# Performance work log

Hardware: AMD Instinct MI355X
Metric: run time of the kernel (lower is better)

## Reference

```python
import jax, jax.numpy as jnp
import numpy as np

B, T, C = 4, 2048, 1024
NQ, D = 8, C // 8  # n_query heads, head dim = n_embd // 8


def setup_inputs() -> dict:
    key = jax.random.key(0)
    ks = jax.random.split(key, 6)
    s = 0.02
    return {
        "x": jax.random.normal(ks[0], (B, T, C), dtype=jnp.float32),
        "Wk": jax.random.normal(ks[1], (C, D), dtype=jnp.float32) * s,
        "Wv": jax.random.normal(ks[2], (C, D), dtype=jnp.float32) * s,
        "Wq": jax.random.normal(ks[3], (NQ, C, D), dtype=jnp.float32) * s,
        "Wp": jax.random.normal(ks[4], (NQ * D, C), dtype=jnp.float32) * s,
        "bp": jnp.zeros((C,), dtype=jnp.float32),
    }


def reference(x, Wk, Wv, Wq, Wp, bp):
    b, t, c = x.shape
    scale = c ** -0.5  # original scales by n_embd**-0.5, not head-dim
    k = x @ Wk                                   # [B,T,D] shared across heads (MQA)
    v = x @ Wv                                   # [B,T,D]
    q = jnp.einsum("btc,qcd->bqtd", x, Wq)       # [B,NQ,T,D]
    wei = jnp.einsum("bqtd,bsd->bqts", q, k) * scale
    causal = jnp.tril(jnp.ones((t, t), dtype=bool))
    wei = jnp.where(causal, wei, -jnp.inf)
    wei = jax.nn.softmax(wei, axis=-1)
    out = jnp.einsum("bqts,bsd->btqd", wei, v)   # [B,T,NQ,D]
    out = out.reshape(b, t, -1)                  # concat heads -> [B,T,NQ*D]
    return out @ Wp + bp
```

## Files before the change

### kernel.cpp

```cpp
#include <hip/hip_runtime.h>
#include <hip/hip_bf16.h>
#include <cstddef>
#include <cstdint>

#define B 4
#define T 2048
#define C 1024
#define NQ 8
#define D 128
#define M_ROWS (B * T)
#define NTOT (2 * D + NQ * D)

typedef __bf16 bf16x8 __attribute__((ext_vector_type(8)));
typedef float  f32x4  __attribute__((ext_vector_type(4)));
typedef uint32_t u32x4 __attribute__((ext_vector_type(4)));

__device__ __forceinline__ ushort f2bf(float f) {
    union { float f; uint32_t u; } v; v.f = f;
    const uint32_t r = (v.u + 0x7fffu + ((v.u >> 16) & 1u)) >> 16;
    return (ushort)r;
}

__device__ __forceinline__ uint32_t cvt_pk_bf16(float lo, float hi) {
    uint32_t r;
    asm("v_cvt_pk_bf16_f32 %0, %1, %2" : "=v"(r) : "v"(lo), "v"(hi));
    return r;
}

__device__ __forceinline__ void gld_lds16(const ushort* g, ushort* lds_uniform) {
    __builtin_amdgcn_global_load_lds(
        (const __attribute__((address_space(1))) void*)g,
        (__attribute__((address_space(3))) void*)lds_uniform, 16, 0, 0);
}

__global__ __launch_bounds__(256) void xcvt(const float* __restrict__ x,
                                            ushort* __restrict__ xb) {
    const size_t i = ((size_t)blockIdx.x * 256 + threadIdx.x) * 8;
    const float4 a = *(const float4*)(x + i);
    const float4 b = *(const float4*)(x + i + 4);
    uint4 o;
    o.x = f2bf(a.x) | ((uint32_t)f2bf(a.y) << 16);
    o.y = f2bf(a.z) | ((uint32_t)f2bf(a.w) << 16);
    o.z = f2bf(b.x) | ((uint32_t)f2bf(b.y) << 16);
    o.w = f2bf(b.z) | ((uint32_t)f2bf(b.w) << 16);
    *(uint4*)(xb + i) = o;
}

__device__ __forceinline__ void wtrans_body(const float* __restrict__ src,
                                            ushort* __restrict__ dst, int NC,
                                            int bx, int by) {
    __shared__ ushort Ts[64][72];
    const int tid = threadIdx.x;
    const int k0 = by * 64, c0 = bx * 64;
    {
        const int r = tid >> 2, cq = tid & 3;
#pragma unroll
        for (int i = 0; i < 4; ++i) {
            const int cc = cq * 16 + i * 4;
            const float4 v = *(const float4*)(src + (size_t)(k0 + r) * NC + c0 + cc);
            uint2 o;
            o.x = f2bf(v.x) | ((uint32_t)f2bf(v.y) << 16);
            o.y = f2bf(v.z) | ((uint32_t)f2bf(v.w) << 16);
            *(uint2*)(&Ts[r][cc]) = o;
        }
    }
    __syncthreads();
    {
        const int n = tid >> 2, kq = tid & 3;
        ushort vv[16];
#pragma unroll
        for (int j = 0; j < 16; ++j) vv[j] = Ts[kq * 16 + j][n];
        uint4 o0, o1;
        o0.x = vv[0] | ((uint32_t)vv[1] << 16);  o0.y = vv[2] | ((uint32_t)vv[3] << 16);
        o0.z = vv[4] | ((uint32_t)vv[5] << 16);  o0.w = vv[6] | ((uint32_t)vv[7] << 16);
        o1.x = vv[8] | ((uint32_t)vv[9] << 16);  o1.y = vv[10] | ((uint32_t)vv[11] << 16);
        o1.z = vv[12] | ((uint32_t)vv[13] << 16); o1.w = vv[14] | ((uint32_t)vv[15] << 16);
        ushort* d = dst + (size_t)(c0 + n) * C + k0 + kq * 16;
        *(uint4*)d = o0;
        *(uint4*)(d + 8) = o1;
    }
}

__global__ __launch_bounds__(256) void wtrans_qkv(const float* __restrict__ Wk,
                                                  const float* __restrict__ Wv,
                                                  const float* __restrict__ Wq,
                                                  ushort* __restrict__ WcatT) {
    const int z = blockIdx.z;
    const float* src;
    int rbase;
    if (z == 0)      { src = Wk; rbase = 0; }
    else if (z == 1) { src = Wv; rbase = D; }
    else             { src = Wq + (size_t)(z - 2) * C * D; rbase = 2 * D + (z - 2) * D; }
    wtrans_body(src, WcatT + (size_t)rbase * C, D, blockIdx.x, blockIdx.y);
}

__global__ __launch_bounds__(256) void wtrans_p(const float* __restrict__ Wp,
                                                ushort* __restrict__ WpT) {
    wtrans_body(Wp, WpT, C, blockIdx.x, blockIdx.y);
}

__global__ __launch_bounds__(256) void vtrans(const ushort* __restrict__ qkv,
                                              ushort* __restrict__ vbT) {
    __shared__ ushort Ts[64][136];
    const int tid = threadIdx.x;
    const int kb0 = blockIdx.x * 64;
    {
        const int r = tid >> 2, cq = tid & 3;
        const ushort* src = qkv + (size_t)(kb0 + r) * NTOT + D;
#pragma unroll
        for (int i = 0; i < 4; ++i) {
            const int cc = (cq * 4 + i) * 8;
            *(uint4*)(&Ts[r][cc]) = *(const uint4*)(src + cc);
        }
    }
    __syncthreads();
    {
        const int d = tid >> 1, half = tid & 1;
        ushort vv[32];
#pragma unroll
        for (int k = 0; k < 32; ++k) vv[k] = Ts[half * 32 + k][d];
        uint32_t dw[16];
#pragma unroll
        for (int i = 0; i < 16; ++i) {
            const int p0 = 2 * i, p1 = 2 * i + 1;
            const int k0 = (p0 & 3) | (((p0 >> 3) & 3) << 2) | (((p0 >> 2) & 1) << 4);
            const int k1 = (p1 & 3) | (((p1 >> 3) & 3) << 2) | (((p1 >> 2) & 1) << 4);
            dw[i] = vv[k0] | ((uint32_t)vv[k1] << 16);
        }
        uint32_t* dst = (uint32_t*)(vbT + (size_t)d * M_ROWS + kb0 + half * 32);
#pragma unroll
        for (int i = 0; i < 4; ++i)
            *(uint4*)(dst + i * 4) = *(uint4*)(&dw[i * 4]);
    }
}

template <bool BF16_OUT>
__global__ __launch_bounds__(256) void gemm_mfma(const ushort* __restrict__ A,
                                                 const ushort* __restrict__ Bt,
                                                 void* __restrict__ Cout,
                                                 const float* __restrict__ bias,
                                                 const int Nout) {
    __shared__ ushort As[128 * 32];
    __shared__ ushort Bs[128 * 32];
    const int tid  = threadIdx.x;
    const int lane = tid & 63;
    const int w    = tid >> 6;
    const int col  = lane & 15;
    const int quad = lane >> 4;
    const int row0 = blockIdx.y * 128;
    const int col0 = blockIdx.x * 128;
    const int wm = w & 1, wn = w >> 1;

    const int srow = lane >> 2;
    const int skk  = (lane & 3) * 8;

    f32x4 acc[4][4];
#pragma unroll
    for (int i = 0; i < 4; ++i)
#pragma unroll
        for (int j = 0; j < 4; ++j) acc[i][j] = (f32x4){0.f, 0.f, 0.f, 0.f};

    for (int k0 = 0; k0 < C; k0 += 32) {
        __syncthreads();
#pragma unroll
        for (int j = 0; j < 2; ++j) {
            const int ci = w * 2 + j;
            const int r  = ci * 16 + srow;
            gld_lds16(A  + (size_t)(row0 + r) * C + k0 + skk, &As[ci * 512]);
            gld_lds16(Bt + (size_t)(col0 + r) * C + k0 + skk, &Bs[ci * 512]);
        }
        __syncthreads();

        bf16x8 af[4], bfr[4];
#pragma unroll
        for (int i = 0; i < 4; ++i)
            af[i] = *(const bf16x8*)&As[(wm * 64 + i * 16 + col) * 32 + quad * 8];
#pragma unroll
        for (int j = 0; j < 4; ++j)
            bfr[j] = *(const bf16x8*)&Bs[(wn * 64 + j * 16 + col) * 32 + quad * 8];
#pragma unroll
        for (int i = 0; i < 4; ++i)
#pragma unroll
            for (int j = 0; j < 4; ++j)
                acc[i][j] = __builtin_amdgcn_mfma_f32_16x16x32_bf16(af[i], bfr[j], acc[i][j], 0, 0, 0);
    }

#pragma unroll
    for (int i = 0; i < 4; ++i) {
#pragma unroll
        for (int r = 0; r < 4; ++r) {
            const int grow = row0 + wm * 64 + i * 16 + quad * 4 + r;
#pragma unroll
            for (int j = 0; j < 4; ++j) {
                const int gcol = col0 + wn * 64 + j * 16 + col;
                const float v = acc[i][j][r];
                if (BF16_OUT) {
                    ((ushort*)Cout)[(size_t)grow * Nout + gcol] = f2bf(v);
                } else {
                    ((float*)Cout)[(size_t)grow * Nout + gcol] = v + bias[gcol];
                }
            }
        }
    }
}

__global__ __launch_bounds__(128, 2) void attn_mfma(const ushort* __restrict__ qkv,
                                                    const ushort* __restrict__ vbT,
                                                    ushort* __restrict__ attb) {
    __shared__ ushort Ks4[4][64][32];
    __shared__ ushort Vt4[4][128][16];

    const int tid  = threadIdx.x;
    const int lane = tid & 63;
    const int w    = tid >> 6;
    const int col  = lane & 15;
    const int quad = lane >> 4;
    const int h    = blockIdx.y;
    const int b    = blockIdx.z;
    const int qb_i = (b & 1) ? (gridDim.x - 1 - blockIdx.x) : blockIdx.x;
    const int q0   = qb_i * 64;

    bf16x8 qf[2][4];
#pragma unroll
    for (int qs = 0; qs < 2; ++qs) {
        const ushort* qrow = qkv + (size_t)(b * T + q0 + w * 32 + qs * 16 + col) * NTOT + 2 * D + h * D;
#pragma unroll
        for (int kb2 = 0; kb2 < 4; ++kb2)
            qf[qs][kb2] = *(const bf16x8*)(qrow + kb2 * 32 + quad * 8);
    }

    const ushort* kbase = qkv + (size_t)b * T * NTOT;
    const ushort* vbase = vbT + (size_t)b * T;

    f32x4 O[2][8];
#pragma unroll
    for (int qs = 0; qs < 2; ++qs)
#pragma unroll
        for (int i = 0; i < 8; ++i) O[qs][i] = (f32x4){0.f, 0.f, 0.f, 0.f};
    float l_acc[2] = {0.f, 0.f};

    const int ntiles  = qb_i + 1;
    const int sk_key  = lane >> 2;
    const int sk_d    = (lane & 3) * 8;
    const int sv_d    = lane >> 1;
    const int sv_half = (lane & 1) * 8;
    const int kg0     = quad >> 1;
    const int ko      = (quad & 1) * 8;
    const float SC = 0.045084220f;

    for (int it = 0; it < ntiles; ++it) {
        const int s0 = it * 64;
        __syncthreads();
#pragma unroll
        for (int cc = 0; cc < 2; ++cc) {
            const int c = w * 2 + cc;
#pragma unroll
            for (int kg = 0; kg < 4; ++kg)
                gld_lds16(kbase + (size_t)(s0 + kg * 16 + sk_key) * NTOT + c * 32 + sk_d,
                          &Ks4[c][kg * 16][0]);
#pragma unroll
            for (int i2 = 0; i2 < 4; ++i2)
                gld_lds16(vbase + (size_t)(i2 * 32 + sv_d) * M_ROWS + s0 + c * 16 + sv_half,
                          &Vt4[c][i2 * 32][0]);
        }
        __syncthreads();

        f32x4 S[2][4];
#pragma unroll
        for (int qs = 0; qs < 2; ++qs)
#pragma unroll
            for (int sub = 0; sub < 4; ++sub) S[qs][sub] = (f32x4){0.f, 0.f, 0.f, 0.f};
#pragma unroll
        for (int sub = 0; sub < 4; ++sub) {
#pragma unroll
            for (int kb2 = 0; kb2 < 4; ++kb2) {
                bf16x8 kf = *(const bf16x8*)(&Ks4[kb2][sub * 16 + col][quad * 8]);
                S[0][sub] = __builtin_amdgcn_mfma_f32_16x16x32_bf16(kf, qf[0][kb2], S[0][sub], 0, 0, 0);
                S[1][sub] = __builtin_amdgcn_mfma_f32_16x16x32_bf16(kf, qf[1][kb2], S[1][sub], 0, 0, 0);
            }
        }

        const bool diag = (it == ntiles - 1);
        bf16x8 paf[2][2];
#pragma unroll
        for (int qs = 0; qs < 2; ++qs) {
            float p[4][4];
            if (diag) {
                const int q = q0 + w * 32 + qs * 16 + col;
#pragma unroll
                for (int sub = 0; sub < 4; ++sub)
#pragma unroll
                    for (int r = 0; r < 4; ++r) {
                        const int key = s0 + sub * 16 + quad * 4 + r;
                        const float sc = (key > q) ? -1e30f : S[qs][sub][r] * SC;
                        p[sub][r] = __builtin_amdgcn_exp2f(sc);
                    }
            } else {
#pragma unroll
                for (int sub = 0; sub < 4; ++sub)
#pragma unroll
                    for (int r = 0; r < 4; ++r)
                        p[sub][r] = __builtin_amdgcn_exp2f(S[qs][sub][r] * SC);
            }
            float ls = 0.f;
#pragma unroll
            for (int sub = 0; sub < 4; ++sub)
                ls += (p[sub][0] + p[sub][1]) + (p[sub][2] + p[sub][3]);
            l_acc[qs] += ls;

            u32x4 w0, w1;
            w0.x = cvt_pk_bf16(p[0][0], p[0][1]);
            w0.y = cvt_pk_bf16(p[0][2], p[0][3]);
            w0.z = cvt_pk_bf16(p[1][0], p[1][1]);
            w0.w = cvt_pk_bf16(p[1][2], p[1][3]);
            w1.x = cvt_pk_bf16(p[2][0], p[2][1]);
            w1.y = cvt_pk_bf16(p[2][2], p[2][3]);
            w1.z = cvt_pk_bf16(p[3][0], p[3][1]);
            w1.w = cvt_pk_bf16(p[3][2], p[3][3]);
            paf[qs][0] = __builtin_bit_cast(bf16x8, w0);
            paf[qs][1] = __builtin_bit_cast(bf16x8, w1);
        }

#pragma unroll
        for (int nt = 0; nt < 8; ++nt) {
            bf16x8 vf0 = *(const bf16x8*)(&Vt4[kg0][nt * 16 + col][ko]);
            bf16x8 vf1 = *(const bf16x8*)(&Vt4[2 + kg0][nt * 16 + col][ko]);
#pragma unroll
            for (int qs = 0; qs < 2; ++qs) {
                O[qs][nt] = __builtin_amdgcn_mfma_f32_16x16x32_bf16(paf[qs][0], vf0, O[qs][nt], 0, 0, 0);
                O[qs][nt] = __builtin_amdgcn_mfma_f32_16x16x32_bf16(paf[qs][1], vf1, O[qs][nt], 0, 0, 0);
            }
        }
    }

#pragma unroll
    for (int qs = 0; qs < 2; ++qs) {
        float s = l_acc[qs];
        s += __shfl_xor(s, 16);
        s += __shfl_xor(s, 32);
#pragma unroll
        for (int r = 0; r < 4; ++r) {
            const float inv = 1.0f / __shfl(s, quad * 4 + r);
            const int t = q0 + w * 32 + qs * 16 + quad * 4 + r;
            ushort* orow = attb + (size_t)(b * T + t) * C + h * D;
#pragma unroll
            for (int nt = 0; nt < 8; ++nt)
                orow[nt * 16 + col] = f2bf(O[qs][nt][r] * inv);
        }
    }
}

extern "C" void kernel_launch(void* const* d_in, const int* in_sizes, int n_in,
                              void* d_out, int out_size, void* d_ws, size_t ws_size,
                              hipStream_t stream) {
    const float* x  = (const float*)d_in[0];
    const float* Wk = (const float*)d_in[1];
    const float* Wv = (const float*)d_in[2];
    const float* Wq = (const float*)d_in[3];
    const float* Wp = (const float*)d_in[4];
    const float* bp = (const float*)d_in[5];
    float* out = (float*)d_out;

    char* ws = (char*)d_ws;
    ushort* xb    = (ushort*)ws;
    ushort* attb  = xb;
    ushort* qkv   = (ushort*)(ws + (size_t)16  * 1024 * 1024);
    ushort* WcatT = (ushort*)(ws + (size_t)36  * 1024 * 1024);
    ushort* WpT   = (ushort*)(ws + (size_t)39  * 1024 * 1024);
    ushort* vbT   = (ushort*)(ws + (size_t)41  * 1024 * 1024);

    xcvt<<<(size_t)M_ROWS * C / (256 * 8), 256, 0, stream>>>(x, xb);
    wtrans_qkv<<<dim3(D / 64, C / 64, 2 + NQ), 256, 0, stream>>>(Wk, Wv, Wq, WcatT);
    wtrans_p<<<dim3(C / 64, C / 64), 256, 0, stream>>>(Wp, WpT);

    gemm_mfma<true><<<dim3(NTOT / 128, M_ROWS / 128), 256, 0, stream>>>(
        xb, WcatT, qkv, nullptr, NTOT);

    vtrans<<<M_ROWS / 64, 256, 0, stream>>>(qkv, vbT);

    attn_mfma<<<dim3(T / 64, NQ, B), 128, 0, stream>>>(qkv, vbT, attb);

    gemm_mfma<false><<<dim3(C / 128, M_ROWS / 128), 256, 0, stream>>>(
        attb, WpT, out, bp, C);
}
```

Baseline: 227.7 us.

## Double-buffer K/V tiles in attention and grow query block to 128 rows

The attention kernel now runs 256 threads per block, each block covering 128 query rows with four waves, and K/V tiles are double-buffered in LDS. The next tile is prefetched before compute, so one barrier per iteration replaces two and loads overlap the MFMA work. Each K/V tile is also reused by twice as many query rows. In exchange the kernel uses twice the LDS, launches half as many blocks, and the first two waves sit idle on the last tile because it is fully masked for them.

```diff
diff --git a/kernel.cpp b/kernel.cpp
--- a/kernel.cpp
+++ b/kernel.cpp
@@ -204,11 +204,11 @@
     }
 }
 
-__global__ __launch_bounds__(128, 2) void attn_mfma(const ushort* __restrict__ qkv,
+__global__ __launch_bounds__(256, 2) void attn_mfma(const ushort* __restrict__ qkv,
                                                     const ushort* __restrict__ vbT,
                                                     ushort* __restrict__ attb) {
-    __shared__ ushort Ks4[4][64][32];
-    __shared__ ushort Vt4[4][128][16];
+    __shared__ ushort Ks[2][4][64][32];
+    __shared__ ushort Vt[2][4][128][16];
 
     const int tid  = threadIdx.x;
     const int lane = tid & 63;
@@ -217,8 +217,8 @@
     const int quad = lane >> 4;
     const int h    = blockIdx.y;
     const int b    = blockIdx.z;
-    const int qb_i = (b & 1) ? (gridDim.x - 1 - blockIdx.x) : blockIdx.x;
-    const int q0   = qb_i * 64;
+    const int qb_i = ((b >> 1) & 1) ? (gridDim.x - 1 - blockIdx.x) : blockIdx.x;
+    const int q0   = qb_i * 128;
 
     bf16x8 qf[2][4];
 #pragma unroll
@@ -239,7 +239,7 @@
         for (int i = 0; i < 8; ++i) O[qs][i] = (f32x4){0.f, 0.f, 0.f, 0.f};
     float l_acc[2] = {0.f, 0.f};
 
-    const int ntiles  = qb_i + 1;
+    const int ntiles  = 2 * qb_i + 2;
     const int sk_key  = lane >> 2;
     const int sk_d    = (lane & 3) * 8;
     const int sv_d    = lane >> 1;
@@ -248,89 +248,99 @@
     const int ko      = (quad & 1) * 8;
     const float SC = 0.045084220f;
 
+    auto stage = [&](int it, int bufi) {
+        const int s0 = it * 64;
+#pragma unroll
+        for (int kg = 0; kg < 4; ++kg)
+            gld_lds16(kbase + (size_t)(s0 + kg * 16 + sk_key) * NTOT + w * 32 + sk_d,
+                      &Ks[bufi][w][kg * 16][0]);
+#pragma unroll
+        for (int i2 = 0; i2 < 4; ++i2)
+            gld_lds16(vbase + (size_t)(i2 * 32 + sv_d) * M_ROWS + s0 + w * 16 + sv_half,
+                      &Vt[bufi][w][i2 * 32][0]);
+    };
+
+    int cur = 0;
+    stage(0, 0);
+    __syncthreads();
+
     for (int it = 0; it < ntiles; ++it) {
-        const int s0 = it * 64;
+        if (it + 1 < ntiles) stage(it + 1, cur ^ 1);
+
+        const bool active = (w >= 2) || (it < ntiles - 1);
+        if (active) {
+            const int s0 = it * 64;
+
+            f32x4 S[2][4];
+#pragma unroll
+            for (int qs = 0; qs < 2; ++qs)
+#pragma unroll
+                for (int sub = 0; sub < 4; ++sub) S[qs][sub] = (f32x4){0.f, 0.f, 0.f, 0.f};
+#pragma unroll
+            for (int sub = 0; sub < 4; ++sub) {
+#pragma unroll
+                for (int kb2 = 0; kb2 < 4; ++kb2) {
+                    bf16x8 kf = *(const bf16x8*)(&Ks[cur][kb2][sub * 16 + col][quad * 8]);
+                    S[0][sub] = __builtin_amdgcn_mfma_f32_16x16x32_bf16(kf, qf[0][kb2], S[0][sub], 0, 0, 0);
+                    S[1][sub] = __builtin_amdgcn_mfma_f32_16x16x32_bf16(kf, qf[1][kb2], S[1][sub], 0, 0, 0);
+                }
+            }
+
+            const bool diag = (it >= ntiles - 2);
+            bf16x8 paf[2][2];
+#pragma unroll
+            for (int qs = 0; qs < 2; ++qs) {
+                float p[4][4];
+                if (diag) {
+                    const int q = q0 + w * 32 + qs * 16 + col;
+#pragma unroll
+                    for (int sub = 0; sub < 4; ++sub)
+#pragma unroll
+                        for (int r = 0; r < 4; ++r) {
+                            const int key = s0 + sub * 16 + quad * 4 + r;
+                            const float sc = (key > q) ? -1e30f : S[qs][sub][r] * SC;
+                            p[sub][r] = __builtin_amdgcn_exp2f(sc);
+                        }
+                } else {
+#pragma unroll
+                    for (int sub = 0; sub < 4; ++sub)
+#pragma unroll
+                        for (int r = 0; r < 4; ++r)
+                            p[sub][r] = __builtin_amdgcn_exp2f(S[qs][sub][r] * SC);
+                }
+                float ls = 0.f;
+#pragma unroll
+                for (int sub = 0; sub < 4; ++sub)
+                    ls += (p[sub][0] + p[sub][1]) + (p[sub][2] + p[sub][3]);
+                l_acc[qs] += ls;
+
+                u32x4 w0, w1;
+                w0.x = cvt_pk_bf16(p[0][0], p[0][1]);
+                w0.y = cvt_pk_bf16(p[0][2], p[0][3]);
+                w0.z = cvt_pk_bf16(p[1][0], p[1][1]);
+                w0.w = cvt_pk_bf16(p[1][2], p[1][3]);
+                w1.x = cvt_pk_bf16(p[2][0], p[2][1]);
+                w1.y = cvt_pk_bf16(p[2][2], p[2][3]);
+                w1.z = cvt_pk_bf16(p[3][0], p[3][1]);
+                w1.w = cvt_pk_bf16(p[3][2], p[3][3]);
+                paf[qs][0] = __builtin_bit_cast(bf16x8, w0);
+                paf[qs][1] = __builtin_bit_cast(bf16x8, w1);
+            }
+
+#pragma unroll
+            for (int nt = 0; nt < 8; ++nt) {
+                bf16x8 vf0 = *(const bf16x8*)(&Vt[cur][kg0][nt * 16 + col][ko]);
+                bf16x8 vf1 = *(const bf16x8*)(&Vt[cur][2 + kg0][nt * 16 + col][ko]);
+#pragma unroll
+                for (int qs = 0; qs < 2; ++qs) {
+                    O[qs][nt] = __builtin_amdgcn_mfma_f32_16x16x32_bf16(paf[qs][0], vf0, O[qs][nt], 0, 0, 0);
+                    O[qs][nt] = __builtin_amdgcn_mfma_f32_16x16x32_bf16(paf[qs][1], vf1, O[qs][nt], 0, 0, 0);
+                }
+            }
+        }
+
         __syncthreads();
-#pragma unroll
-        for (int cc = 0; cc < 2; ++cc) {
-            const int c = w * 2 + cc;
-#pragma unroll
-            for (int kg = 0; kg < 4; ++kg)
-                gld_lds16(kbase + (size_t)(s0 + kg * 16 + sk_key) * NTOT + c * 32 + sk_d,
-                          &Ks4[c][kg * 16][0]);
-#pragma unroll
-            for (int i2 = 0; i2 < 4; ++i2)
-                gld_lds16(vbase + (size_t)(i2 * 32 + sv_d) * M_ROWS + s0 + c * 16 + sv_half,
-                          &Vt4[c][i2 * 32][0]);
-        }
-        __syncthreads();
-
-        f32x4 S[2][4];
-#pragma unroll
-        for (int qs = 0; qs < 2; ++qs)
-#pragma unroll
-            for (int sub = 0; sub < 4; ++sub) S[qs][sub] = (f32x4){0.f, 0.f, 0.f, 0.f};
-#pragma unroll
-        for (int sub = 0; sub < 4; ++sub) {
-#pragma unroll
-            for (int kb2 = 0; kb2 < 4; ++kb2) {
-                bf16x8 kf = *(const bf16x8*)(&Ks4[kb2][sub * 16 + col][quad * 8]);
-                S[0][sub] = __builtin_amdgcn_mfma_f32_16x16x32_bf16(kf, qf[0][kb2], S[0][sub], 0, 0, 0);
-                S[1][sub] = __builtin_amdgcn_mfma_f32_16x16x32_bf16(kf, qf[1][kb2], S[1][sub], 0, 0, 0);
-            }
-        }
-
-        const bool diag = (it == ntiles - 1);
-        bf16x8 paf[2][2];
-#pragma unroll
-        for (int qs = 0; qs < 2; ++qs) {
-            float p[4][4];
-            if (diag) {
-                const int q = q0 + w * 32 + qs * 16 + col;
-#pragma unroll
-                for (int sub = 0; sub < 4; ++sub)
-#pragma unroll
-                    for (int r = 0; r < 4; ++r) {
-                        const int key = s0 + sub * 16 + quad * 4 + r;
-                        const float sc = (key > q) ? -1e30f : S[qs][sub][r] * SC;
-                        p[sub][r] = __builtin_amdgcn_exp2f(sc);
-                    }
-            } else {
-#pragma unroll
-                for (int sub = 0; sub < 4; ++sub)
-#pragma unroll
-                    for (int r = 0; r < 4; ++r)
-                        p[sub][r] = __builtin_amdgcn_exp2f(S[qs][sub][r] * SC);
-            }
-            float ls = 0.f;
-#pragma unroll
-            for (int sub = 0; sub < 4; ++sub)
-                ls += (p[sub][0] + p[sub][1]) + (p[sub][2] + p[sub][3]);
-            l_acc[qs] += ls;
-
-            u32x4 w0, w1;
-            w0.x = cvt_pk_bf16(p[0][0], p[0][1]);
-            w0.y = cvt_pk_bf16(p[0][2], p[0][3]);
-            w0.z = cvt_pk_bf16(p[1][0], p[1][1]);
-            w0.w = cvt_pk_bf16(p[1][2], p[1][3]);
-            w1.x = cvt_pk_bf16(p[2][0], p[2][1]);
-            w1.y = cvt_pk_bf16(p[2][2], p[2][3]);
-            w1.z = cvt_pk_bf16(p[3][0], p[3][1]);
-            w1.w = cvt_pk_bf16(p[3][2], p[3][3]);
-            paf[qs][0] = __builtin_bit_cast(bf16x8, w0);
-            paf[qs][1] = __builtin_bit_cast(bf16x8, w1);
-        }
-
-#pragma unroll
-        for (int nt = 0; nt < 8; ++nt) {
-            bf16x8 vf0 = *(const bf16x8*)(&Vt4[kg0][nt * 16 + col][ko]);
-            bf16x8 vf1 = *(const bf16x8*)(&Vt4[2 + kg0][nt * 16 + col][ko]);
-#pragma unroll
-            for (int qs = 0; qs < 2; ++qs) {
-                O[qs][nt] = __builtin_amdgcn_mfma_f32_16x16x32_bf16(paf[qs][0], vf0, O[qs][nt], 0, 0, 0);
-                O[qs][nt] = __builtin_amdgcn_mfma_f32_16x16x32_bf16(paf[qs][1], vf1, O[qs][nt], 0, 0, 0);
-            }
-        }
+        cur ^= 1;
     }
 
 #pragma unroll
@@ -378,7 +388,7 @@
 
     vtrans<<<M_ROWS / 64, 256, 0, stream>>>(qkv, vbT);
 
-    attn_mfma<<<dim3(T / 64, NQ, B), 128, 0, stream>>>(qkv, vbT, attb);
+    attn_mfma<<<dim3(T / 128, NQ, B), 256, 0, stream>>>(qkv, vbT, attb);
 
     gemm_mfma<false><<<dim3(C / 128, M_ROWS / 128), 256, 0, stream>>>(
         attb, WpT, out, bp, C);
```

New measurement: 211.6 us. 1.08x faster.

## Load K and V fragments directly from global memory, dropping LDS staging in attention

Applied to the files above, without the earlier changes.

The attention kernel no longer stages K and V tiles through shared memory with barriers. Each wave now reads its MFMA operand fragments straight from global memory (relying on L1/L2 caching), which removes both __syncthreads per tile and the LDS footprint. It also changes the block-to-query-tile mapping so batches 2 and 3 rotate the order by half, aiming to balance causal work across CUs. The cost is redundant global and cache traffic, since both waves and all heads reload the same K/V with strided, less coalesced accesses.

```diff
diff --git a/kernel.cpp b/kernel.cpp
--- a/kernel.cpp
+++ b/kernel.cpp
@@ -207,9 +207,6 @@
 __global__ __launch_bounds__(128, 2) void attn_mfma(const ushort* __restrict__ qkv,
                                                     const ushort* __restrict__ vbT,
                                                     ushort* __restrict__ attb) {
-    __shared__ ushort Ks4[4][64][32];
-    __shared__ ushort Vt4[4][128][16];
-
     const int tid  = threadIdx.x;
     const int lane = tid & 63;
     const int w    = tid >> 6;
@@ -217,20 +214,21 @@
     const int quad = lane >> 4;
     const int h    = blockIdx.y;
     const int b    = blockIdx.z;
-    const int qb_i = (b & 1) ? (gridDim.x - 1 - blockIdx.x) : blockIdx.x;
-    const int q0   = qb_i * 64;
+    const int xr   = (b & 1) ? (31 - (int)blockIdx.x) : (int)blockIdx.x;
+    const int qb   = (b & 2) ? ((xr + 16) & 31) : xr;
+    const int q0   = qb * 64 + w * 32;
 
     bf16x8 qf[2][4];
 #pragma unroll
     for (int qs = 0; qs < 2; ++qs) {
-        const ushort* qrow = qkv + (size_t)(b * T + q0 + w * 32 + qs * 16 + col) * NTOT + 2 * D + h * D;
+        const ushort* qrow = qkv + (size_t)(b * T + q0 + qs * 16 + col) * NTOT + 2 * D + h * D;
 #pragma unroll
         for (int kb2 = 0; kb2 < 4; ++kb2)
             qf[qs][kb2] = *(const bf16x8*)(qrow + kb2 * 32 + quad * 8);
     }
 
-    const ushort* kbase = qkv + (size_t)b * T * NTOT;
-    const ushort* vbase = vbT + (size_t)b * T;
+    const ushort* kb_ = qkv + (size_t)b * T * NTOT + quad * 8;
+    const ushort* vb_ = vbT + (size_t)b * T;
 
     f32x4 O[2][8];
 #pragma unroll
@@ -239,31 +237,12 @@
         for (int i = 0; i < 8; ++i) O[qs][i] = (f32x4){0.f, 0.f, 0.f, 0.f};
     float l_acc[2] = {0.f, 0.f};
 
-    const int ntiles  = qb_i + 1;
-    const int sk_key  = lane >> 2;
-    const int sk_d    = (lane & 3) * 8;
-    const int sv_d    = lane >> 1;
-    const int sv_half = (lane & 1) * 8;
-    const int kg0     = quad >> 1;
-    const int ko      = (quad & 1) * 8;
+    const int ntiles = qb + 1;
     const float SC = 0.045084220f;
 
     for (int it = 0; it < ntiles; ++it) {
         const int s0 = it * 64;
-        __syncthreads();
-#pragma unroll
-        for (int cc = 0; cc < 2; ++cc) {
-            const int c = w * 2 + cc;
-#pragma unroll
-            for (int kg = 0; kg < 4; ++kg)
-                gld_lds16(kbase + (size_t)(s0 + kg * 16 + sk_key) * NTOT + c * 32 + sk_d,
-                          &Ks4[c][kg * 16][0]);
-#pragma unroll
-            for (int i2 = 0; i2 < 4; ++i2)
-                gld_lds16(vbase + (size_t)(i2 * 32 + sv_d) * M_ROWS + s0 + c * 16 + sv_half,
-                          &Vt4[c][i2 * 32][0]);
-        }
-        __syncthreads();
+        const ushort* krow = kb_ + (size_t)s0 * NTOT;
 
         f32x4 S[2][4];
 #pragma unroll
@@ -272,11 +251,14 @@
             for (int sub = 0; sub < 4; ++sub) S[qs][sub] = (f32x4){0.f, 0.f, 0.f, 0.f};
 #pragma unroll
         for (int sub = 0; sub < 4; ++sub) {
+            bf16x8 kf[4];
+#pragma unroll
+            for (int kb2 = 0; kb2 < 4; ++kb2)
+                kf[kb2] = *(const bf16x8*)(krow + (size_t)(sub * 16 + col) * NTOT + kb2 * 32);
 #pragma unroll
             for (int kb2 = 0; kb2 < 4; ++kb2) {
-                bf16x8 kf = *(const bf16x8*)(&Ks4[kb2][sub * 16 + col][quad * 8]);
-                S[0][sub] = __builtin_amdgcn_mfma_f32_16x16x32_bf16(kf, qf[0][kb2], S[0][sub], 0, 0, 0);
-                S[1][sub] = __builtin_amdgcn_mfma_f32_16x16x32_bf16(kf, qf[1][kb2], S[1][sub], 0, 0, 0);
+                S[0][sub] = __builtin_amdgcn_mfma_f32_16x16x32_bf16(kf[kb2], qf[0][kb2], S[0][sub], 0, 0, 0);
+                S[1][sub] = __builtin_amdgcn_mfma_f32_16x16x32_bf16(kf[kb2], qf[1][kb2], S[1][sub], 0, 0, 0);
             }
         }
 
@@ -286,7 +268,7 @@
         for (int qs = 0; qs < 2; ++qs) {
             float p[4][4];
             if (diag) {
-                const int q = q0 + w * 32 + qs * 16 + col;
+                const int q = q0 + qs * 16 + col;
 #pragma unroll
                 for (int sub = 0; sub < 4; ++sub)
 #pragma unroll
@@ -323,12 +305,13 @@
 
 #pragma unroll
         for (int nt = 0; nt < 8; ++nt) {
-            bf16x8 vf0 = *(const bf16x8*)(&Vt4[kg0][nt * 16 + col][ko]);
-            bf16x8 vf1 = *(const bf16x8*)(&Vt4[2 + kg0][nt * 16 + col][ko]);
+            const ushort* vrow = vb_ + (size_t)(nt * 16 + col) * M_ROWS + s0 + quad * 8;
+            const bf16x8 vfa = *(const bf16x8*)(vrow);
+            const bf16x8 vfb = *(const bf16x8*)(vrow + 32);
 #pragma unroll
             for (int qs = 0; qs < 2; ++qs) {
-                O[qs][nt] = __builtin_amdgcn_mfma_f32_16x16x32_bf16(paf[qs][0], vf0, O[qs][nt], 0, 0, 0);
-                O[qs][nt] = __builtin_amdgcn_mfma_f32_16x16x32_bf16(paf[qs][1], vf1, O[qs][nt], 0, 0, 0);
+                O[qs][nt] = __builtin_amdgcn_mfma_f32_16x16x32_bf16(paf[qs][0], vfa, O[qs][nt], 0, 0, 0);
+                O[qs][nt] = __builtin_amdgcn_mfma_f32_16x16x32_bf16(paf[qs][1], vfb, O[qs][nt], 0, 0, 0);
             }
         }
     }
@@ -341,7 +324,7 @@
 #pragma unroll
         for (int r = 0; r < 4; ++r) {
             const float inv = 1.0f / __shfl(s, quad * 4 + r);
-            const int t = q0 + w * 32 + qs * 16 + quad * 4 + r;
+            const int t = q0 + qs * 16 + quad * 4 + r;
             ushort* orow = attb + (size_t)(b * T + t) * C + h * D;
 #pragma unroll
             for (int nt = 0; nt < 8; ++nt)
```

Measured after the change: 323.0 us. +41.9%, slower.
